# Performance work log

Measured on AMD Instinct MI355X. Metric: run time of the kernel, lower is better.

## Reference

```python
import jax, jax.numpy as jnp
import numpy as np

B, S, H, NH = 2, 2048, 2048, 16
HD = H // NH  # 128
NEG = -1e9


def _rope_tables(seq_len, dim, dtype):
    inv_freq = 1.0 / (10000.0 ** (jnp.arange(0, dim, 2, dtype=jnp.float32) / dim))
    t = jnp.arange(seq_len, dtype=jnp.float32)
    freqs = jnp.einsum('i,j->ij', t, inv_freq)          # [S, dim/2]
    emb = jnp.concatenate([freqs, freqs], axis=-1)      # [S, dim]
    return jnp.cos(emb).astype(dtype), jnp.sin(emb).astype(dtype)


def _rotate_half(x):
    x1, x2 = x[..., : x.shape[-1] // 2], x[..., x.shape[-1] // 2:]
    return jnp.concatenate([-x2, x1], axis=-1)


def setup_inputs() -> dict:
    key = jax.random.key(0)
    ks = jax.random.split(key, 5)
    hidden_states = jax.random.normal(ks[0], (B, S, H), dtype=jnp.float32)
    # causal additive mask [B, S, S]
    causal = jnp.where(jnp.tril(jnp.ones((S, S), dtype=bool)), 0.0, NEG).astype(jnp.float32)
    attention_mask = jnp.broadcast_to(causal, (B, S, S))
    sc = 1.0 / np.sqrt(H)
    Wq = jax.random.normal(ks[1], (H, H), dtype=jnp.float32) * sc
    Wk = jax.random.normal(ks[2], (H, H), dtype=jnp.float32) * sc
    Wv = jax.random.normal(ks[3], (H, H), dtype=jnp.float32) * sc
    Wo = jax.random.normal(ks[4], (H, H), dtype=jnp.float32) * sc
    return {"hidden_states": hidden_states, "attention_mask": attention_mask,
            "Wq": Wq, "Wk": Wk, "Wv": Wv, "Wo": Wo}


def reference(hidden_states, attention_mask, Wq, Wk, Wv, Wo):
    bsz, q_len, _ = hidden_states.shape
    dtype = hidden_states.dtype
    # QKV projections (nn.Linear: x @ W.T), split into heads -> [B, NH, S, HD]
    def proj(W):
        return jnp.einsum('bsh,dh->bsd', hidden_states, W).reshape(bsz, q_len, NH, HD).transpose(0, 2, 1, 3)
    q, k, v = proj(Wq), proj(Wk), proj(Wv)
    cos, sin = _rope_tables(q_len, HD, dtype)            # [S, HD]
    q = q * cos + _rotate_half(q) * sin
    k = k * cos + _rotate_half(k) * sin
    scaling = HD ** -0.5
    scores = jnp.einsum('bhqd,bhkd->bhqk', q, k) * scaling
    scores = scores + attention_mask[:, None, :, :]      # broadcast over heads
    attn = jax.nn.softmax(scores.astype(jnp.float32), axis=-1).astype(dtype)
    out = jnp.einsum('bhqk,bhkd->bhqd', attn, v)         # [B, NH, S, HD]
    out = out.transpose(0, 2, 1, 3).reshape(bsz, q_len, H)
    return jnp.einsum('bsh,dh->bsd', out, Wo)
```

## Files before the change

kernel.cpp:

```cpp
#include <hip/hip_runtime.h>
#include <hip/hip_bf16.h>
#include <math.h>

#define B_  2
#define S_  2048
#define H_  2048
#define NH_ 16
#define HD_ 128
#define M_  (B_*S_)

typedef __bf16 bf16_t;
typedef _Float16 f16_t;
typedef __bf16 bf16x8 __attribute__((ext_vector_type(8)));
typedef __bf16 bf16x4 __attribute__((ext_vector_type(4)));
typedef _Float16 f16x4 __attribute__((ext_vector_type(4)));
typedef float  f32x4  __attribute__((ext_vector_type(4)));

__device__ __forceinline__ f32x4 mfma_bf16_32(bf16x8 a, bf16x8 b, f32x4 c) {
  return __builtin_amdgcn_mfma_f32_16x16x32_bf16(a, b, c, 0, 0, 0);
}
__device__ __forceinline__ f32x4 mfma_f16_16(f16x4 a, f16x4 b, f32x4 c) {
  return __builtin_amdgcn_mfma_f32_16x16x16f16(a, b, c, 0, 0, 0);
}
__device__ __forceinline__ void gl_lds16(const void* g, void* l) {
  __builtin_amdgcn_global_load_lds((const __attribute__((address_space(1))) void*)g,
                                   (__attribute__((address_space(3))) void*)l, 16, 0, 0);
}
#define WAITCNT_VM(n) { asm volatile("" ::: "memory"); \
                        __builtin_amdgcn_s_waitcnt(((n) & 0xF) | 0x70 | 0xF00 | (((n) >> 4) << 14)); \
                        asm volatile("" ::: "memory"); }
#define BARRIER()     { asm volatile("" ::: "memory"); __builtin_amdgcn_s_barrier(); \
                        asm volatile("" ::: "memory"); }

__global__ void cvt_all(const float* __restrict__ hs, const float* __restrict__ wq,
                        const float* __restrict__ wk, const float* __restrict__ wv,
                        const float* __restrict__ wo, bf16_t* __restrict__ hs_b,
                        bf16_t* __restrict__ wqkv, bf16_t* __restrict__ wo_b) {
  for (int slot = blockIdx.x * 256 + threadIdx.x; slot < 6291456; slot += 524288) {
    int i = slot * 4;
    const float* src;
    bf16_t* dst;
    if (i < 8388608)        { src = hs + i;              dst = hs_b + i; }
    else if (i < 12582912)  { src = wq + (i - 8388608);  dst = wqkv + (i - 8388608); }
    else if (i < 16777216)  { src = wk + (i - 12582912); dst = wqkv + (i - 8388608); }
    else if (i < 20971520)  { src = wv + (i - 16777216); dst = wqkv + (i - 8388608); }
    else                    { src = wo + (i - 20971520); dst = wo_b + (i - 20971520); }
    float4 v = *(const float4*)src;
    bf16x4 o;
    o[0] = (bf16_t)v.x; o[1] = (bf16_t)v.y; o[2] = (bf16_t)v.z; o[3] = (bf16_t)v.w;
    *(bf16x4*)dst = o;
  }
}

template<int MODE>
__global__ __launch_bounds__(256, 3)
void gemm_mfma(const bf16_t* __restrict__ A, const bf16_t* __restrict__ Bt,
               bf16_t* __restrict__ outQ, bf16_t* __restrict__ outK,
               f16_t* __restrict__ outV, float* __restrict__ outF, int K) {
  __shared__ bf16_t sA[128 * 64];
  __shared__ bf16_t sB[128 * 64];
  const int tid  = threadIdx.x;
  const int lane = tid & 63;
  const int w    = tid >> 6;
  const int col  = lane & 15;
  const int quad = lane >> 4;
  const int w_m  = (w & 1) * 64;
  const int w_n2 = (w >> 1) * 32;
  const int m_blk = blockIdx.y * 128;
  const int n_blk = blockIdx.x * 128;

  const int srow   = lane >> 3;
  const int schunk = (lane & 7) ^ (lane >> 3);

  const bf16_t* Abase = A  + (size_t)m_blk * K;
  const bf16_t* Bbase = Bt + (size_t)n_blk * K;

  f32x4 acc[4][4] = {};

  for (int kk = 0; kk < K; kk += 64) {
    __syncthreads();
#pragma unroll
    for (int p = 0; p < 4; ++p) {
      int seg = w * 4 + p;
      int row = seg * 8 + srow;
      gl_lds16(Abase + (size_t)row * K + kk + schunk * 8, &sA[seg * 512]);
      gl_lds16(Bbase + (size_t)row * K + kk + schunk * 8, &sB[seg * 512]);
    }
    __syncthreads();
#pragma unroll
    for (int kc = 0; kc < 2; ++kc) {
      bf16x8 af[4], bfr[4];
      const int cs = (kc * 4 + quad) ^ (col & 7);
#pragma unroll
      for (int i = 0; i < 4; ++i) {
        af[i]  = *(const bf16x8*)&sA[(w_m + i * 16 + col) * 64 + cs * 8];
        bfr[i] = *(const bf16x8*)&sB[(w_n2 + (i & 1) * 16 + (i >> 1) * 64 + col) * 64 + cs * 8];
      }
#pragma unroll
      for (int mi = 0; mi < 4; ++mi)
#pragma unroll
        for (int ni = 0; ni < 4; ++ni)
          acc[mi][ni] = mfma_bf16_32(af[mi], bfr[ni], acc[mi][ni]);
    }
  }

  const int sel = n_blk >> 11;
  if (MODE == 0 && sel == 2) {
#pragma unroll
    for (int mi = 0; mi < 4; ++mi)
#pragma unroll
      for (int ni = 0; ni < 4; ++ni) {
        int m0 = m_blk + w_m + mi * 16 + quad * 4;
        int n  = n_blk + w_n2 + (ni & 1) * 16 + (ni >> 1) * 64 + col;
        int n_l = n & (H_ - 1);
        int head = n_l >> 7, hd = n_l & (HD_ - 1);
        int b = m0 >> 11, s0 = m0 & (S_ - 1);
        int bh = b * NH_ + head;
        int frag = (bh * 32 + (s0 >> 6)) * 32 + (hd >> 4) * 4 + ((s0 >> 4) & 3);
        int lane2 = ((s0 >> 2) & 3) * 16 + (hd & 15);
        f16x4 o;
#pragma unroll
        for (int r = 0; r < 4; ++r) o[r] = (f16_t)acc[mi][ni][r];
        *(f16x4*)&outV[(size_t)frag * 256 + lane2 * 4] = o;
      }
  } else if (MODE == 0) {
    const float kscale = 0.12751744154f;
    const int head = (n_blk & (H_ - 1)) >> 7;
#pragma unroll
    for (int ni = 0; ni < 2; ++ni) {
      const int d = w_n2 + ni * 16 + col;
      const float rf = exp2f(-(float)d * 0.20762050593046f - 2.6514961294723187f);
#pragma unroll
      for (int mi = 0; mi < 4; ++mi) {
#pragma unroll
        for (int r = 0; r < 4; ++r) {
          int m = m_blk + w_m + mi * 16 + quad * 4 + r;
          int b = m >> 11, s = m & (S_ - 1);
          int bh = b * NH_ + head;
          float rev = (float)s * rf;
          rev -= floorf(rev);
          float cc = __builtin_amdgcn_cosf(rev);
          float sn = __builtin_amdgcn_sinf(rev);
          float x1 = acc[mi][ni][r], x2 = acc[mi][ni + 2][r];
          float o1 = x1 * cc - x2 * sn;
          float o2 = x2 * cc + x1 * sn;
          if (sel == 0) {
            bf16_t* qwr = outQ + ((size_t)bh * S_ + s) * HD_;
            qwr[d]      = (bf16_t)o1;
            qwr[d + 64] = (bf16_t)o2;
          } else {
            int kt = s >> 6, t = (s >> 4) & 3;
            int lane_ = ((d >> 3) & 3) * 16 + (s & 15);
            bf16_t* kbase = outK + ((size_t)(bh * 32 + kt) * 16) * 512;
            kbase[(size_t)(t * 4 + (d >> 5)) * 512 + lane_ * 8 + (d & 7)]     = (bf16_t)(o1 * kscale);
            kbase[(size_t)(t * 4 + (d >> 5) + 2) * 512 + lane_ * 8 + (d & 7)] = (bf16_t)(o2 * kscale);
          }
        }
      }
    }
  } else {
#pragma unroll
    for (int mi = 0; mi < 4; ++mi)
#pragma unroll
      for (int ni = 0; ni < 4; ++ni)
#pragma unroll
        for (int r = 0; r < 4; ++r) {
          int m = m_blk + w_m + mi * 16 + quad * 4 + r;
          int n = n_blk + w_n2 + (ni & 1) * 16 + (ni >> 1) * 64 + col;
          outF[(size_t)m * H_ + n] = acc[mi][ni][r];
        }
  }
}

__global__ __launch_bounds__(256, 4)
void flash_attn(const bf16_t* __restrict__ Q, const bf16_t* __restrict__ Kp,
                const f16_t* __restrict__ Vp, bf16_t* __restrict__ Out) {
  __shared__ bf16_t sK[8192];
  __shared__ f16_t  sV[8192];
  const int lane = threadIdx.x & 63;
  const int col  = lane & 15;
  const int quad = lane >> 4;
  const int w    = threadIdx.x >> 6;

  const int c = blockIdx.x & 7, g = blockIdx.x >> 3;
  const int g2 = (g + (blockIdx.y >> 3)) & 3;
  const int qt = (g2 == 0) ? c : (g2 == 1) ? 15 - c : (g2 == 2) ? 16 + c : 31 - c;
  const int bh = blockIdx.y;
  const int ktmax = qt;

  const bf16_t* KpB = Kp + (size_t)bh * 32 * 8192;
  const f16_t*  VpB = Vp + (size_t)bh * 32 * 8192;

  auto stageK = [&](int kt) {
#pragma unroll
    for (int r = 0; r < 4; ++r) {
      int seg = r * 4 + w;
      gl_lds16(KpB + (size_t)kt * 8192 + seg * 512 + lane * 8, &sK[seg * 512]);
    }
  };
  auto stageV = [&](int kt) {
#pragma unroll
    for (int r = 0; r < 4; ++r) {
      int seg = r * 4 + w;
      gl_lds16(VpB + (size_t)kt * 8192 + seg * 512 + lane * 8, &sV[seg * 512]);
    }
  };

  const bf16_t* Qrow = Q + ((size_t)bh * S_ + qt * 64 + w * 16 + col) * HD_;
  bf16x8 qf[4];
#pragma unroll
  for (int kc = 0; kc < 4; ++kc)
    qf[kc] = *(const bf16x8*)(Qrow + kc * 32 + quad * 8);

  f32x4 oacc[8] = {};
  float m_i = -1e30f, l_i = 0.f;

  stageK(0);
  stageV(0);
  WAITCNT_VM(4)
  BARRIER();

  for (int kt = 0; kt <= ktmax; ++kt) {
    f32x4 st[4] = {};
    __builtin_amdgcn_s_setprio(1);
#pragma unroll
    for (int kc = 0; kc < 4; ++kc)
#pragma unroll
      for (int t = 0; t < 4; ++t) {
        bf16x8 kf = *(const bf16x8*)&sK[(t * 4 + kc) * 512 + lane * 8];
        st[t] = mfma_bf16_32(kf, qf[kc], st[t]);
      }
    __builtin_amdgcn_s_setprio(0);

    if (kt == ktmax) {
      int ql = w * 16 + col;
#pragma unroll
      for (int t = 0; t < 4; ++t)
#pragma unroll
        for (int r = 0; r < 4; ++r)
          if (t * 16 + quad * 4 + r > ql) st[t][r] = -1e30f;
    }

    float pm[4];
#pragma unroll
    for (int t = 0; t < 4; ++t)
      pm[t] = fmaxf(fmaxf(st[t][0], st[t][1]), fmaxf(st[t][2], st[t][3]));
    float mx = fmaxf(fmaxf(pm[0], pm[1]), fmaxf(pm[2], pm[3]));
    mx = fmaxf(mx, __shfl_xor(mx, 16, 64));
    mx = fmaxf(mx, __shfl_xor(mx, 32, 64));
    if (__ballot(mx - m_i > 8.0f)) {
      float mn = fmaxf(m_i, mx);
      float alpha = exp2f(m_i - mn);
#pragma unroll
      for (int dt = 0; dt < 8; ++dt)
#pragma unroll
        for (int r = 0; r < 4; ++r) oacc[dt][r] *= alpha;
      l_i *= alpha;
      m_i = mn;
    }

    f16x4 pf[4];
    float ts[4];
#pragma unroll
    for (int t = 0; t < 4; ++t) {
      float a = exp2f(st[t][0] - m_i);
      float b2 = exp2f(st[t][1] - m_i);
      float cc = exp2f(st[t][2] - m_i);
      float d2 = exp2f(st[t][3] - m_i);
      pf[t][0] = (f16_t)a; pf[t][1] = (f16_t)b2;
      pf[t][2] = (f16_t)cc; pf[t][3] = (f16_t)d2;
      ts[t] = (a + b2) + (cc + d2);
    }
    float sum = (ts[0] + ts[1]) + (ts[2] + ts[3]);
    sum += __shfl_xor(sum, 16, 64);
    sum += __shfl_xor(sum, 32, 64);
    l_i += sum;

    WAITCNT_VM(0)
    BARRIER();

    if (kt < ktmax) stageK(kt + 1);

    __builtin_amdgcn_s_setprio(1);
#pragma unroll
    for (int t = 0; t < 4; ++t)
#pragma unroll
      for (int dt = 0; dt < 8; ++dt) {
        f16x4 vf = *(const f16x4*)&sV[(dt * 4 + t) * 256 + lane * 4];
        oacc[dt] = mfma_f16_16(vf, pf[t], oacc[dt]);
      }
    __builtin_amdgcn_s_setprio(0);

    if (kt < ktmax) {
      BARRIER();
      stageV(kt + 1);
      WAITCNT_VM(4)
      BARRIER();
    }
  }

  float inv = 1.0f / l_i;
  int b = bh >> 4, h = bh & (NH_ - 1);
  int qg = qt * 64 + w * 16 + col;
  bf16_t* Orow = Out + ((size_t)b * S_ + qg) * H_ + h * HD_;
#pragma unroll
  for (int dt = 0; dt < 8; ++dt) {
    bf16x4 o4;
#pragma unroll
    for (int r = 0; r < 4; ++r) o4[r] = (bf16_t)(oacc[dt][r] * inv);
    *(bf16x4*)(Orow + dt * 16 + quad * 4) = o4;
  }
}

extern "C" void kernel_launch(void* const* d_in, const int* in_sizes, int n_in,
                              void* d_out, int out_size, void* d_ws, size_t ws_size,
                              hipStream_t stream) {
  const float* hs = (const float*)d_in[0];
  const float* Wq = (const float*)d_in[2];
  const float* Wk = (const float*)d_in[3];
  const float* Wv = (const float*)d_in[4];
  const float* Wo = (const float*)d_in[5];
  float* out = (float*)d_out;

  char* ws = (char*)d_ws;
  size_t off = 0;
  auto alloc = [&](size_t bytes) -> void* {
    void* p = ws + off;
    off += (bytes + 255) & ~(size_t)255;
    return p;
  };
  bf16_t* hs_b  = (bf16_t*)alloc((size_t)M_ * H_ * 2);
  bf16_t* wqkv  = (bf16_t*)alloc((size_t)3 * H_ * H_ * 2);
  bf16_t* wo_b  = (bf16_t*)alloc((size_t)H_ * H_ * 2);
  bf16_t* Qbuf  = (bf16_t*)alloc((size_t)M_ * H_ * 2);
  bf16_t* Kp    = (bf16_t*)alloc((size_t)M_ * H_ * 2);
  f16_t*  Vp    = (f16_t*)alloc((size_t)M_ * H_ * 2);
  bf16_t* attn  = (bf16_t*)alloc((size_t)M_ * H_ * 2);

  cvt_all<<<2048, 256, 0, stream>>>(hs, Wq, Wk, Wv, Wo, hs_b, wqkv, wo_b);

  gemm_mfma<0><<<dim3(48, 32), 256, 0, stream>>>(hs_b, wqkv, Qbuf, Kp,
                                                 Vp, nullptr, H_);

  flash_attn<<<dim3(32, 32), 256, 0, stream>>>(Qbuf, Kp, Vp, attn);

  gemm_mfma<1><<<dim3(16, 32), 256, 0, stream>>>(attn, wo_b, nullptr, nullptr,
                                                 nullptr, out, H_);
}
```

Baseline: 375.8 us.

## Load K/V fragments directly from global memory instead of staging through LDS

Drops the LDS staging of K and V tiles, along with the async global-to-LDS loads, waitcnts and block barriers. Each wave now reads its pre-packed K and V fragments straight from global memory into registers before the MFMAs. This removes barrier synchronisation and LDS traffic. In exchange, the four waves of a block each fetch the same K/V tile separately and rely on cache hits, and global load latency is exposed with no explicit prefetch.

```diff
diff --git a/kernel.cpp b/kernel.cpp
--- a/kernel.cpp
+++ b/kernel.cpp
@@ -26,11 +26,6 @@
   __builtin_amdgcn_global_load_lds((const __attribute__((address_space(1))) void*)g,
                                    (__attribute__((address_space(3))) void*)l, 16, 0, 0);
 }
-#define WAITCNT_VM(n) { asm volatile("" ::: "memory"); \
-                        __builtin_amdgcn_s_waitcnt(((n) & 0xF) | 0x70 | 0xF00 | (((n) >> 4) << 14)); \
-                        asm volatile("" ::: "memory"); }
-#define BARRIER()     { asm volatile("" ::: "memory"); __builtin_amdgcn_s_barrier(); \
-                        asm volatile("" ::: "memory"); }
 
 __global__ void cvt_all(const float* __restrict__ hs, const float* __restrict__ wq,
                         const float* __restrict__ wk, const float* __restrict__ wv,
@@ -175,8 +170,6 @@
 __global__ __launch_bounds__(256, 4)
 void flash_attn(const bf16_t* __restrict__ Q, const bf16_t* __restrict__ Kp,
                 const f16_t* __restrict__ Vp, bf16_t* __restrict__ Out) {
-  __shared__ bf16_t sK[8192];
-  __shared__ f16_t  sV[8192];
   const int lane = threadIdx.x & 63;
   const int col  = lane & 15;
   const int quad = lane >> 4;
@@ -188,23 +181,8 @@
   const int bh = blockIdx.y;
   const int ktmax = qt;
 
-  const bf16_t* KpB = Kp + (size_t)bh * 32 * 8192;
-  const f16_t*  VpB = Vp + (size_t)bh * 32 * 8192;
-
-  auto stageK = [&](int kt) {
-#pragma unroll
-    for (int r = 0; r < 4; ++r) {
-      int seg = r * 4 + w;
-      gl_lds16(KpB + (size_t)kt * 8192 + seg * 512 + lane * 8, &sK[seg * 512]);
-    }
-  };
-  auto stageV = [&](int kt) {
-#pragma unroll
-    for (int r = 0; r < 4; ++r) {
-      int seg = r * 4 + w;
-      gl_lds16(VpB + (size_t)kt * 8192 + seg * 512 + lane * 8, &sV[seg * 512]);
-    }
-  };
+  const bf16_t* KpL = Kp + (size_t)bh * 32 * 8192 + lane * 8;
+  const f16_t*  VpL = Vp + (size_t)bh * 32 * 8192 + lane * 4;
 
   const bf16_t* Qrow = Q + ((size_t)bh * S_ + qt * 64 + w * 16 + col) * HD_;
   bf16x8 qf[4];
@@ -215,22 +193,23 @@
   f32x4 oacc[8] = {};
   float m_i = -1e30f, l_i = 0.f;
 
-  stageK(0);
-  stageV(0);
-  WAITCNT_VM(4)
-  BARRIER();
-
   for (int kt = 0; kt <= ktmax; ++kt) {
+    const bf16_t* Kt = KpL + (size_t)kt * 8192;
+    const f16_t*  Vt = VpL + (size_t)kt * 8192;
+
     f32x4 st[4] = {};
-    __builtin_amdgcn_s_setprio(1);
-#pragma unroll
-    for (int kc = 0; kc < 4; ++kc)
-#pragma unroll
-      for (int t = 0; t < 4; ++t) {
-        bf16x8 kf = *(const bf16x8*)&sK[(t * 4 + kc) * 512 + lane * 8];
-        st[t] = mfma_bf16_32(kf, qf[kc], st[t]);
-      }
-    __builtin_amdgcn_s_setprio(0);
+#pragma unroll
+    for (int kc = 0; kc < 4; ++kc) {
+      bf16x8 kf[4];
+#pragma unroll
+      for (int t = 0; t < 4; ++t)
+        kf[t] = *(const bf16x8*)(Kt + (t * 4 + kc) * 512);
+      __builtin_amdgcn_s_setprio(1);
+#pragma unroll
+      for (int t = 0; t < 4; ++t)
+        st[t] = mfma_bf16_32(kf[t], qf[kc], st[t]);
+      __builtin_amdgcn_s_setprio(0);
+    }
 
     if (kt == ktmax) {
       int ql = w * 16 + col;
@@ -276,26 +255,17 @@
     sum += __shfl_xor(sum, 32, 64);
     l_i += sum;
 
-    WAITCNT_VM(0)
-    BARRIER();
-
-    if (kt < ktmax) stageK(kt + 1);
-
-    __builtin_amdgcn_s_setprio(1);
-#pragma unroll
-    for (int t = 0; t < 4; ++t)
-#pragma unroll
-      for (int dt = 0; dt < 8; ++dt) {
-        f16x4 vf = *(const f16x4*)&sV[(dt * 4 + t) * 256 + lane * 4];
-        oacc[dt] = mfma_f16_16(vf, pf[t], oacc[dt]);
-      }
-    __builtin_amdgcn_s_setprio(0);
-
-    if (kt < ktmax) {
-      BARRIER();
-      stageV(kt + 1);
-      WAITCNT_VM(4)
-      BARRIER();
+#pragma unroll
+    for (int t = 0; t < 4; ++t) {
+      f16x4 vf[8];
+#pragma unroll
+      for (int dt = 0; dt < 8; ++dt)
+        vf[dt] = *(const f16x4*)(Vt + (dt * 4 + t) * 256);
+      __builtin_amdgcn_s_setprio(1);
+#pragma unroll
+      for (int dt = 0; dt < 8; ++dt)
+        oacc[dt] = mfma_f16_16(vf[dt], pf[t], oacc[dt]);
+      __builtin_amdgcn_s_setprio(0);
     }
   }
 
```

After: 429.6 us. +14.3%, slower.
